# Kernel tuning notes

Hardware: AMD Instinct MI355X
Metric: run time of the kernel (lower is better)

## Reference

```python
import jax, jax.numpy as jnp
import numpy as np

N, E, D_IN, D_OUT = 50000, 1600000, 256, 256


def setup_inputs() -> dict:
    key = jax.random.key(0)
    k1, k2, k3, k4, k5, k6 = jax.random.split(key, 6)
    x = jax.random.normal(k1, (N, D_IN), dtype=jnp.float32)
    edge_index = jax.random.randint(k2, (2, E), 0, N, dtype=jnp.int64)
    s = 1.0 / np.sqrt(D_IN)
    W1 = jax.random.uniform(k3, (D_OUT, D_IN), minval=-s, maxval=s, dtype=jnp.float32)
    b1 = jax.random.uniform(k4, (D_OUT,), minval=-s, maxval=s, dtype=jnp.float32)
    W2 = jax.random.uniform(k5, (D_OUT, D_IN), minval=-s, maxval=s, dtype=jnp.float32)
    b2 = jax.random.uniform(k6, (D_OUT,), minval=-s, maxval=s, dtype=jnp.float32)
    return {"x": x, "W1": W1, "b1": b1, "W2": W2, "b2": b2, "edge_index": edge_index}


def reference(x, W1, b1, W2, b2, edge_index):
    # edge_index[0] = destination node, edge_index[1] = neighbor (as in the torch loop)
    dst = edge_index[0]
    nbr = edge_index[1]
    n = x.shape[0]
    # segment mean of neighbor features per destination node
    agg = jax.ops.segment_sum(x[nbr], dst, num_segments=n)  # [N, D_IN]
    cnt = jax.ops.segment_sum(jnp.ones((nbr.shape[0],), x.dtype), dst, num_segments=n)
    mean = agg / jnp.maximum(cnt, 1.0)[:, None]  # isolated nodes -> 0 (torch gives NaN)
    return x @ W1.T + b1 + mean @ W2.T + b2
```

## Files before the change

kernel.cpp:

```cpp
#include <hip/hip_runtime.h>
#include <hip/hip_bf16.h>
#include <hip/hip_fp8.h>

typedef __bf16 bf16x4 __attribute__((ext_vector_type(4)));
typedef __bf16 bf16x8 __attribute__((ext_vector_type(8)));
typedef float f32x4 __attribute__((ext_vector_type(4)));
typedef float f32x2 __attribute__((ext_vector_type(2)));

#define D_IN 256
#define D_OUT 256
#define K_DIM 512
#define PAD 96
#define NBIN 640
#define NPS 79
#define ROUND1 3072
#define CAP3 20
#define CVT_BLK 1024
#define CONVW_BLK 512


__device__ __forceinline__ unsigned int pack4_fp8(float a, float b, float c, float d) {
#if __has_builtin(__builtin_amdgcn_cvt_pk_fp8_f32)
    int r = 0;
    r = __builtin_amdgcn_cvt_pk_fp8_f32(a, b, r, false);
    r = __builtin_amdgcn_cvt_pk_fp8_f32(c, d, r, true);
    return (unsigned int)r;
#else
    union { unsigned int u; unsigned char by[4]; } v;
    v.by[0] = __hip_fp8_e4m3(a).__x;
    v.by[1] = __hip_fp8_e4m3(b).__x;
    v.by[2] = __hip_fp8_e4m3(c).__x;
    v.by[3] = __hip_fp8_e4m3(d).__x;
    return v.u;
#endif
}

__device__ __forceinline__ void unpack4_fp8(unsigned int u, f32x2& lo, f32x2& hi) {
#if __has_builtin(__builtin_amdgcn_cvt_pk_f32_fp8)
    lo = __builtin_amdgcn_cvt_pk_f32_fp8(u, false);
    hi = __builtin_amdgcn_cvt_pk_f32_fp8(u, true);
#else
    union { unsigned int uu; unsigned char by[4]; } v; v.uu = u;
    __hip_fp8_e4m3 q0, q1, q2, q3;
    q0.__x = v.by[0]; q1.__x = v.by[1]; q2.__x = v.by[2]; q3.__x = v.by[3];
    lo[0] = (float)q0; lo[1] = (float)q1; hi[0] = (float)q2; hi[1] = (float)q3;
#endif
}


__global__ __launch_bounds__(256) void prep_kernel(const int* __restrict__ dst,
                                                   unsigned int* __restrict__ hist,
                                                   const float* __restrict__ x,
                                                   unsigned int* __restrict__ x8,
                                                   __bf16* __restrict__ xb,
                                                   const float* __restrict__ W1,
                                                   const float* __restrict__ W2,
                                                   const float* __restrict__ b1,
                                                   const float* __restrict__ b2,
                                                   __bf16* __restrict__ Wbuf,
                                                   float* __restrict__ bias,
                                                   int E, int n8, int nSub) {
    __shared__ int bcnt[NBIN];
    const int tid = threadIdx.x;
    const int bid = blockIdx.x;

    if (bid < nSub) {
        for (int s = tid; s < NBIN; s += 256) bcnt[s] = 0;
        __syncthreads();
        const int base = bid * ROUND1;
        const int hi = min(E, base + ROUND1);
        for (int e = base + tid; e < hi; e += 256) {
            int d = __builtin_nontemporal_load(dst + e);
            atomicAdd(&bcnt[d / NPS], 1);
        }
        __syncthreads();
        for (int s = tid; s < NBIN; s += 256)
            hist[(size_t)bid * NBIN + s] = (unsigned int)bcnt[s];
    } else if (bid < nSub + CVT_BLK) {
        int i = (bid - nSub) * 256 + tid;
        for (; i < n8; i += CVT_BLK * 256) {
            const float4* p = (const float4*)(x + (size_t)i * 8);
            float4 a = p[0], b = p[1];
            uint2 o;
            o.x = pack4_fp8(a.x, a.y, a.z, a.w);
            o.y = pack4_fp8(b.x, b.y, b.z, b.w);
            *(uint2*)(x8 + (size_t)i * 2) = o;
            bf16x8 hb = { (__bf16)a.x, (__bf16)a.y, (__bf16)a.z, (__bf16)a.w,
                          (__bf16)b.x, (__bf16)b.y, (__bf16)b.z, (__bf16)b.w };
            *(bf16x8*)(xb + (size_t)i * 8) = hb;
        }
    } else {
        int i = (bid - nSub - CVT_BLK) * 256 + tid;
        int o = i >> 9;
        int k = i & 511;
        float v = (k < D_IN) ? W1[o * D_IN + k] : W2[o * D_IN + (k - D_IN)];
        Wbuf[i] = (__bf16)v;
        if (i < D_OUT) bias[i] = b1[i] + b2[i];
    }
}


__global__ __launch_bounds__(64) void scan_kernel(const unsigned int* __restrict__ hist,
                                                  unsigned int* __restrict__ sbase,
                                                  int* __restrict__ bin_cnt, int nSub) {
    const int s = blockIdx.x;
    const int lane = threadIdx.x;
    unsigned int carry = 0;
    for (int b0 = 0; b0 < nSub; b0 += 64) {
        int b = b0 + lane;
        unsigned int v = (b < nSub) ? hist[(size_t)b * NBIN + s] : 0u;
        unsigned int sc = v;
        #pragma unroll
        for (int d = 1; d < 64; d <<= 1) {
            unsigned int t = __shfl_up(sc, d, 64);
            if (lane >= d) sc += t;
        }
        if (b < nSub) sbase[(size_t)b * NBIN + s] = carry + sc - v;
        carry += __shfl(sc, 63, 64);
    }
    if (lane == 0) bin_cnt[s] = (int)carry;
}


__global__ __launch_bounds__(256) void place_kernel(const int* __restrict__ dst,
                                                    const int* __restrict__ nbr,
                                                    const unsigned int* __restrict__ sbase,
                                                    unsigned int* __restrict__ bins,
                                                    int E, int segCap, int nSub) {
    __shared__ unsigned int buf[NBIN][CAP3];
    __shared__ int bcnt[NBIN];
    __shared__ unsigned int gbase[NBIN];
    const int tid = threadIdx.x;
    const int bid = blockIdx.x;

    for (int s = tid; s < NBIN; s += 256) {
        bcnt[s] = 0;
        gbase[s] = sbase[(size_t)bid * NBIN + s];
    }
    __syncthreads();

    const int base = bid * ROUND1;
    const int hi = min(E, base + ROUND1);
    for (int e = base + tid; e < hi; e += 256) {
        int d  = __builtin_nontemporal_load(dst + e);
        int nb = __builtin_nontemporal_load(nbr + e);
        int s = d / NPS;
        unsigned int packed = ((unsigned int)d << 16) | (unsigned int)nb;
        int pos = atomicAdd(&bcnt[s], 1);
        if (pos < CAP3) buf[s][pos] = packed;
        else bins[(size_t)s * segCap + gbase[s] + pos] = packed;
    }
    __syncthreads();

    const int wave = tid >> 6, lane = tid & 63;
    for (int s = wave; s < NBIN; s += 4) {
        int c = min(bcnt[s], CAP3);
        if (lane < c) bins[(size_t)s * segCap + gbase[s] + lane] = buf[s][lane];
    }
}


__global__ __launch_bounds__(512) void fillgather_kernel(const unsigned int* __restrict__ x8,
                                                         const unsigned int* __restrict__ bins,
                                                         const int* __restrict__ bin_cnt,
                                                         __bf16* __restrict__ Mbuf,
                                                         int segCap, int N) {
    __shared__ unsigned short lbuck[NPS][PAD];
    __shared__ int lcnt[NPS];
    const int s = blockIdx.x;
    const int node0 = s * NPS;
    const int tid = threadIdx.x;

    for (int i = tid; i < NPS; i += 512) lcnt[i] = 0;
    __syncthreads();

    const int cnt = min(bin_cnt[s], segCap);
    const size_t sbase_ = (size_t)s * segCap;
    for (int i = tid; i < cnt; i += 512) {
        unsigned int p = bins[sbase_ + i];
        int nl = (int)(p >> 16) - node0;
        int pos = atomicAdd(&lcnt[nl], 1);
        if (pos < PAD) lbuck[nl][pos] = (unsigned short)(p & 0xffffu);
    }
    __syncthreads();

    const int wave = tid >> 6, lane = tid & 63;
    for (int nl = wave; nl < NPS; nl += 8) {
        int node = node0 + nl;
        if (node >= N) continue;
        int c = min(lcnt[nl], PAD);
        const unsigned int* bw = (const unsigned int*)(&lbuck[nl][0]);

        f32x2 a0lo = {0.f,0.f}, a0hi = {0.f,0.f};
        f32x2 a1lo = {0.f,0.f}, a1hi = {0.f,0.f};
        f32x2 a2lo = {0.f,0.f}, a2hi = {0.f,0.f};
        f32x2 a3lo = {0.f,0.f}, a3hi = {0.f,0.f};

        int i = 0;
        for (; i + 16 <= c; i += 16) {
            int ib = i >> 1;
            unsigned int w0 = bw[ib+0], w1 = bw[ib+1], w2 = bw[ib+2], w3 = bw[ib+3];
            unsigned int w4 = bw[ib+4], w5 = bw[ib+5], w6 = bw[ib+6], w7 = bw[ib+7];
            unsigned int u0  = x8[(size_t)(w0 & 0xffffu) * 64 + lane];
            unsigned int u1  = x8[(size_t)(w0 >> 16)     * 64 + lane];
            unsigned int u2  = x8[(size_t)(w1 & 0xffffu) * 64 + lane];
            unsigned int u3  = x8[(size_t)(w1 >> 16)     * 64 + lane];
            unsigned int u4  = x8[(size_t)(w2 & 0xffffu) * 64 + lane];
            unsigned int u5  = x8[(size_t)(w2 >> 16)     * 64 + lane];
            unsigned int u6  = x8[(size_t)(w3 & 0xffffu) * 64 + lane];
            unsigned int u7  = x8[(size_t)(w3 >> 16)     * 64 + lane];
            unsigned int u8  = x8[(size_t)(w4 & 0xffffu) * 64 + lane];
            unsigned int u9  = x8[(size_t)(w4 >> 16)     * 64 + lane];
            unsigned int u10 = x8[(size_t)(w5 & 0xffffu) * 64 + lane];
            unsigned int u11 = x8[(size_t)(w5 >> 16)     * 64 + lane];
            unsigned int u12 = x8[(size_t)(w6 & 0xffffu) * 64 + lane];
            unsigned int u13 = x8[(size_t)(w6 >> 16)     * 64 + lane];
            unsigned int u14 = x8[(size_t)(w7 & 0xffffu) * 64 + lane];
            unsigned int u15 = x8[(size_t)(w7 >> 16)     * 64 + lane];
            f32x2 lo, hi;
            unpack4_fp8(u0,  lo, hi); a0lo += lo; a0hi += hi;
            unpack4_fp8(u1,  lo, hi); a1lo += lo; a1hi += hi;
            unpack4_fp8(u2,  lo, hi); a2lo += lo; a2hi += hi;
            unpack4_fp8(u3,  lo, hi); a3lo += lo; a3hi += hi;
            unpack4_fp8(u4,  lo, hi); a0lo += lo; a0hi += hi;
            unpack4_fp8(u5,  lo, hi); a1lo += lo; a1hi += hi;
            unpack4_fp8(u6,  lo, hi); a2lo += lo; a2hi += hi;
            unpack4_fp8(u7,  lo, hi); a3lo += lo; a3hi += hi;
            unpack4_fp8(u8,  lo, hi); a0lo += lo; a0hi += hi;
            unpack4_fp8(u9,  lo, hi); a1lo += lo; a1hi += hi;
            unpack4_fp8(u10, lo, hi); a2lo += lo; a2hi += hi;
            unpack4_fp8(u11, lo, hi); a3lo += lo; a3hi += hi;
            unpack4_fp8(u12, lo, hi); a0lo += lo; a0hi += hi;
            unpack4_fp8(u13, lo, hi); a1lo += lo; a1hi += hi;
            unpack4_fp8(u14, lo, hi); a2lo += lo; a2hi += hi;
            unpack4_fp8(u15, lo, hi); a3lo += lo; a3hi += hi;
        }
        for (; i + 4 <= c; i += 4) {
            int ib = i >> 1;
            unsigned int w0 = bw[ib+0], w1 = bw[ib+1];
            unsigned int u0 = x8[(size_t)(w0 & 0xffffu) * 64 + lane];
            unsigned int u1 = x8[(size_t)(w0 >> 16)     * 64 + lane];
            unsigned int u2 = x8[(size_t)(w1 & 0xffffu) * 64 + lane];
            unsigned int u3 = x8[(size_t)(w1 >> 16)     * 64 + lane];
            f32x2 lo, hi;
            unpack4_fp8(u0, lo, hi); a0lo += lo; a0hi += hi;
            unpack4_fp8(u1, lo, hi); a1lo += lo; a1hi += hi;
            unpack4_fp8(u2, lo, hi); a2lo += lo; a2hi += hi;
            unpack4_fp8(u3, lo, hi); a3lo += lo; a3hi += hi;
        }
        for (; i < c; i++) {
            unsigned int u0 = x8[(size_t)lbuck[nl][i] * 64 + lane];
            f32x2 lo, hi;
            unpack4_fp8(u0, lo, hi); a0lo += lo; a0hi += hi;
        }
        a0lo += a1lo + a2lo + a3lo;
        a0hi += a1hi + a2hi + a3hi;
        float inv = (c > 0) ? 1.0f / (float)c : 0.0f;
        bf16x4 hm = { (__bf16)(a0lo[0] * inv), (__bf16)(a0lo[1] * inv),
                      (__bf16)(a0hi[0] * inv), (__bf16)(a0hi[1] * inv) };
        *(bf16x4*)(Mbuf + (size_t)node * D_IN + lane * 4) = hm;
    }
}


__global__ __launch_bounds__(512, 5) void gemm_kernel(const __bf16* __restrict__ xb,
                                                      const __bf16* __restrict__ Mb,
                                                      const __bf16* __restrict__ W,
                                                      const float* __restrict__ bias,
                                                      float* __restrict__ out, int M) {
    __shared__ __bf16 As[64][40];
    __shared__ __bf16 Ws[256][40];

    const int tid = threadIdx.x;
    const int lane = tid & 63;
    const int wave = tid >> 6;
    const int wr = wave >> 2;
    const int wc = wave & 3;
    const int brow = blockIdx.x * 64;

    f32x4 acc[2][4];
    #pragma unroll
    for (int m = 0; m < 2; m++)
        #pragma unroll
        for (int n = 0; n < 4; n++)
            acc[m][n] = (f32x4){0.f, 0.f, 0.f, 0.f};

    const int lr = lane & 15;
    const int lg8 = (lane >> 4) * 8;

    const int rowA = tid >> 2;
    const int chA  = (tid & 3) * 8;
    const int growA = brow + rowA;
    const bool aOK = (tid < 256) && (growA < M);
    const int rowW0 = tid >> 2;
    const int rowW1 = (512 + tid) >> 2;
    const int chW = (tid & 3) * 8;

    bf16x8 rA = {};
    bf16x8 rW0, rW1;

    if (aOK) rA = *(const bf16x8*)(xb + (size_t)growA * D_IN + chA);
    rW0 = *(const bf16x8*)(W + (size_t)rowW0 * K_DIM + chW);
    rW1 = *(const bf16x8*)(W + (size_t)rowW1 * K_DIM + chW);

    for (int kk = 0; kk < 16; kk++) {
        if (tid < 256) *(bf16x8*)(&As[rowA][chA]) = rA;
        *(bf16x8*)(&Ws[rowW0][chW]) = rW0;
        *(bf16x8*)(&Ws[rowW1][chW]) = rW1;
        __syncthreads();

        if (kk < 15) {
            const int kn = (kk + 1) * 32;
            const __bf16* srcA = (kn < D_IN) ? xb : Mb;
            if (aOK) rA = *(const bf16x8*)(srcA + (size_t)growA * D_IN + (kn & (D_IN - 1)) + chA);
            rW0 = *(const bf16x8*)(W + (size_t)rowW0 * K_DIM + kn + chW);
            rW1 = *(const bf16x8*)(W + (size_t)rowW1 * K_DIM + kn + chW);
        }

        bf16x8 af[2], wf[4];
        #pragma unroll
        for (int m = 0; m < 2; m++) af[m] = *(const bf16x8*)(&As[wr * 32 + m * 16 + lr][lg8]);
        #pragma unroll
        for (int n = 0; n < 4; n++) wf[n] = *(const bf16x8*)(&Ws[wc * 64 + n * 16 + lr][lg8]);

        #pragma unroll
        for (int m = 0; m < 2; m++)
            #pragma unroll
            for (int n = 0; n < 4; n++)
                acc[m][n] = __builtin_amdgcn_mfma_f32_16x16x32_bf16(af[m], wf[n], acc[m][n], 0, 0, 0);
        __syncthreads();
    }

    const int lg = lane >> 4;
    #pragma unroll
    for (int nf = 0; nf < 4; nf++) {
        int col = wc * 64 + nf * 16 + lr;
        float bv = bias[col];
        #pragma unroll
        for (int mf = 0; mf < 2; mf++) {
            int row0 = brow + wr * 32 + mf * 16 + lg * 4;
            #pragma unroll
            for (int j = 0; j < 4; j++) {
                int row = row0 + j;
                if (row < M) out[(size_t)row * D_OUT + col] = acc[mf][nf][j] + bv;
            }
        }
    }
}


extern "C" void kernel_launch(void* const* d_in, const int* in_sizes, int n_in,
                              void* d_out, int out_size, void* d_ws, size_t ws_size,
                              hipStream_t stream) {
    const float* x  = (const float*)d_in[0];
    const float* W1 = (const float*)d_in[1];
    const float* b1 = (const float*)d_in[2];
    const float* W2 = (const float*)d_in[3];
    const float* b2 = (const float*)d_in[4];
    const int* edges = (const int*)d_in[5];

    const int N = in_sizes[0] / D_IN;
    const int E = in_sizes[5] / 2;
    const int* dst = edges;
    const int* nbr = edges + E;
    const int segCap = (E / NBIN) * 3 / 2 + 64;
    const int nSub = (E + ROUND1 - 1) / ROUND1;
    const int n8 = N * D_IN / 8;

    char* ws = (char*)d_ws;
    size_t woff = 0;
    auto alloc = [&](size_t bytes) -> void* {
        void* p = ws + woff;
        woff = (woff + bytes + 255) & ~(size_t)255;
        return p;
    };
    unsigned int* x8 = (unsigned int*)alloc((size_t)N * D_IN);
    __bf16* xb   = (__bf16*)alloc((size_t)N * D_IN * 2);
    __bf16* Mbuf = (__bf16*)alloc((size_t)N * D_IN * 2);
    __bf16* Wbuf = (__bf16*)alloc((size_t)D_OUT * K_DIM * 2);
    float*  bias = (float*)alloc(D_OUT * 4);
    int* bin_cnt = (int*)alloc(NBIN * 4);
    unsigned int* hist  = (unsigned int*)alloc((size_t)nSub * NBIN * 4);
    unsigned int* sbase = (unsigned int*)alloc((size_t)nSub * NBIN * 4);
    unsigned int* bins  = (unsigned int*)alloc((size_t)NBIN * segCap * 4);

    prep_kernel<<<nSub + CVT_BLK + CONVW_BLK, 256, 0, stream>>>(
        dst, hist, x, x8, xb, W1, W2, b1, b2, Wbuf, bias, E, n8, nSub);
    scan_kernel<<<NBIN, 64, 0, stream>>>(hist, sbase, bin_cnt, nSub);
    place_kernel<<<nSub, 256, 0, stream>>>(dst, nbr, sbase, bins, E, segCap, nSub);

    int fgBlocks = (N + NPS - 1) / NPS;
    fillgather_kernel<<<fgBlocks, 512, 0, stream>>>(x8, bins, bin_cnt, Mbuf, segCap, N);

    int nblk = (N + 63) / 64;
    gemm_kernel<<<nblk, 512, 0, stream>>>(xb, Mbuf, Wbuf, bias, (float*)d_out, N);
}
```

Before: 170.7 us.

## Split GEMM and overlap x@W1 half with edge placement in one launch

Splits the fused K=512 GEMM into two halves. The x@W1 half (plus bias) runs as extra blocks inside the edge-placement kernel, so the dense matmul overlaps with the memory-bound scatter. The mean@W2 half runs after the gather and accumulates into the output by read-modify-write. The placement path moves to 512 threads with a smaller per-bin LDS buffer (CAP3 20->12) so both roles fit one shared-memory layout, at the cost of an extra pass reading and writing the output.

```diff
diff --git a/kernel.cpp b/kernel.cpp
--- a/kernel.cpp
+++ b/kernel.cpp
@@ -14,7 +14,7 @@
 #define NBIN 640
 #define NPS 79
 #define ROUND1 3072
-#define CAP3 20
+#define CAP3 12
 #define CVT_BLK 1024
 #define CONVW_BLK 512
 
@@ -122,40 +122,125 @@
 }
 
 
-__global__ __launch_bounds__(256) void place_kernel(const int* __restrict__ dst,
-                                                    const int* __restrict__ nbr,
-                                                    const unsigned int* __restrict__ sbase,
-                                                    unsigned int* __restrict__ bins,
-                                                    int E, int segCap, int nSub) {
-    __shared__ unsigned int buf[NBIN][CAP3];
-    __shared__ int bcnt[NBIN];
-    __shared__ unsigned int gbase[NBIN];
+__global__ __launch_bounds__(512) void placegemm1_kernel(const int* __restrict__ dst,
+                                                         const int* __restrict__ nbr,
+                                                         const unsigned int* __restrict__ sbase,
+                                                         unsigned int* __restrict__ bins,
+                                                         const __bf16* __restrict__ xb,
+                                                         const __bf16* __restrict__ W,
+                                                         const float* __restrict__ bias,
+                                                         float* __restrict__ out,
+                                                         int E, int segCap, int nSub,
+                                                         int M, int g1) {
+    __shared__ __align__(16) char smem[35840];
     const int tid = threadIdx.x;
     const int bid = blockIdx.x;
 
-    for (int s = tid; s < NBIN; s += 256) {
-        bcnt[s] = 0;
-        gbase[s] = sbase[(size_t)bid * NBIN + s];
-    }
-    __syncthreads();
-
-    const int base = bid * ROUND1;
-    const int hi = min(E, base + ROUND1);
-    for (int e = base + tid; e < hi; e += 256) {
-        int d  = __builtin_nontemporal_load(dst + e);
-        int nb = __builtin_nontemporal_load(nbr + e);
-        int s = d / NPS;
-        unsigned int packed = ((unsigned int)d << 16) | (unsigned int)nb;
-        int pos = atomicAdd(&bcnt[s], 1);
-        if (pos < CAP3) buf[s][pos] = packed;
-        else bins[(size_t)s * segCap + gbase[s] + pos] = packed;
-    }
-    __syncthreads();
-
-    const int wave = tid >> 6, lane = tid & 63;
-    for (int s = wave; s < NBIN; s += 4) {
-        int c = min(bcnt[s], CAP3);
-        if (lane < c) bins[(size_t)s * segCap + gbase[s] + lane] = buf[s][lane];
+    if (bid < g1) {
+        __bf16 (*As)[40] = (__bf16(*)[40])smem;
+        __bf16 (*Ws)[40] = (__bf16(*)[40])(smem + 5120);
+
+        const int lane = tid & 63;
+        const int wave = tid >> 6;
+        const int wr = wave >> 2;
+        const int wc = wave & 3;
+        const int brow = bid * 64;
+
+        f32x4 acc[2][4];
+        #pragma unroll
+        for (int m = 0; m < 2; m++)
+            #pragma unroll
+            for (int n = 0; n < 4; n++)
+                acc[m][n] = (f32x4){0.f, 0.f, 0.f, 0.f};
+
+        const int lr = lane & 15;
+        const int lg8 = (lane >> 4) * 8;
+        const int rowA = tid >> 2;
+        const int chA  = (tid & 3) * 8;
+        const int growA = brow + rowA;
+        const bool aOK = (tid < 256) && (growA < M);
+        const int rowW0 = tid >> 2;
+        const int rowW1 = (512 + tid) >> 2;
+        const int chW = (tid & 3) * 8;
+
+        bf16x8 rA = {};
+        bf16x8 rW0, rW1;
+        if (aOK) rA = *(const bf16x8*)(xb + (size_t)growA * D_IN + chA);
+        rW0 = *(const bf16x8*)(W + (size_t)rowW0 * K_DIM + chW);
+        rW1 = *(const bf16x8*)(W + (size_t)rowW1 * K_DIM + chW);
+
+        for (int kk = 0; kk < 8; kk++) {
+            if (tid < 256) *(bf16x8*)(&As[rowA][chA]) = rA;
+            *(bf16x8*)(&Ws[rowW0][chW]) = rW0;
+            *(bf16x8*)(&Ws[rowW1][chW]) = rW1;
+            __syncthreads();
+
+            if (kk < 7) {
+                const int kn = (kk + 1) * 32;
+                if (aOK) rA = *(const bf16x8*)(xb + (size_t)growA * D_IN + kn + chA);
+                rW0 = *(const bf16x8*)(W + (size_t)rowW0 * K_DIM + kn + chW);
+                rW1 = *(const bf16x8*)(W + (size_t)rowW1 * K_DIM + kn + chW);
+            }
+
+            bf16x8 af[2], wf[4];
+            #pragma unroll
+            for (int m = 0; m < 2; m++) af[m] = *(const bf16x8*)(&As[wr * 32 + m * 16 + lr][lg8]);
+            #pragma unroll
+            for (int n = 0; n < 4; n++) wf[n] = *(const bf16x8*)(&Ws[wc * 64 + n * 16 + lr][lg8]);
+
+            #pragma unroll
+            for (int m = 0; m < 2; m++)
+                #pragma unroll
+                for (int n = 0; n < 4; n++)
+                    acc[m][n] = __builtin_amdgcn_mfma_f32_16x16x32_bf16(af[m], wf[n], acc[m][n], 0, 0, 0);
+            __syncthreads();
+        }
+
+        const int lg = lane >> 4;
+        #pragma unroll
+        for (int nf = 0; nf < 4; nf++) {
+            int col = wc * 64 + nf * 16 + lr;
+            float bv = bias[col];
+            #pragma unroll
+            for (int mf = 0; mf < 2; mf++) {
+                int row0 = brow + wr * 32 + mf * 16 + lg * 4;
+                #pragma unroll
+                for (int j = 0; j < 4; j++) {
+                    int row = row0 + j;
+                    if (row < M) out[(size_t)row * D_OUT + col] = acc[mf][nf][j] + bv;
+                }
+            }
+        }
+    } else {
+        unsigned int (*buf)[CAP3] = (unsigned int(*)[CAP3])smem;
+        int* bcnt = (int*)(smem + 30720);
+        unsigned int* gbase = (unsigned int*)(smem + 33280);
+        const int pbid = bid - g1;
+
+        for (int s = tid; s < NBIN; s += 512) {
+            bcnt[s] = 0;
+            gbase[s] = sbase[(size_t)pbid * NBIN + s];
+        }
+        __syncthreads();
+
+        const int base = pbid * ROUND1;
+        const int hi = min(E, base + ROUND1);
+        for (int e = base + tid; e < hi; e += 512) {
+            int d  = __builtin_nontemporal_load(dst + e);
+            int nb = __builtin_nontemporal_load(nbr + e);
+            int s = d / NPS;
+            unsigned int packed = ((unsigned int)d << 16) | (unsigned int)nb;
+            int pos = atomicAdd(&bcnt[s], 1);
+            if (pos < CAP3) buf[s][pos] = packed;
+            else bins[(size_t)s * segCap + gbase[s] + pos] = packed;
+        }
+        __syncthreads();
+
+        const int wave = tid >> 6, lane = tid & 63;
+        for (int s = wave; s < NBIN; s += 8) {
+            int c = min(bcnt[s], CAP3);
+            if (lane < c) bins[(size_t)s * segCap + gbase[s] + lane] = buf[s][lane];
+        }
     }
 }
 
@@ -263,11 +348,9 @@
 }
 
 
-__global__ __launch_bounds__(512, 5) void gemm_kernel(const __bf16* __restrict__ xb,
-                                                      const __bf16* __restrict__ Mb,
-                                                      const __bf16* __restrict__ W,
-                                                      const float* __restrict__ bias,
-                                                      float* __restrict__ out, int M) {
+__global__ __launch_bounds__(512, 5) void gemm2_kernel(const __bf16* __restrict__ Mb,
+                                                       const __bf16* __restrict__ W,
+                                                       float* __restrict__ out, int M) {
     __shared__ __bf16 As[64][40];
     __shared__ __bf16 Ws[256][40];
 
@@ -287,7 +370,6 @@
 
     const int lr = lane & 15;
     const int lg8 = (lane >> 4) * 8;
-
     const int rowA = tid >> 2;
     const int chA  = (tid & 3) * 8;
     const int growA = brow + rowA;
@@ -298,23 +380,21 @@
 
     bf16x8 rA = {};
     bf16x8 rW0, rW1;
-
-    if (aOK) rA = *(const bf16x8*)(xb + (size_t)growA * D_IN + chA);
-    rW0 = *(const bf16x8*)(W + (size_t)rowW0 * K_DIM + chW);
-    rW1 = *(const bf16x8*)(W + (size_t)rowW1 * K_DIM + chW);
-
-    for (int kk = 0; kk < 16; kk++) {
+    if (aOK) rA = *(const bf16x8*)(Mb + (size_t)growA * D_IN + chA);
+    rW0 = *(const bf16x8*)(W + (size_t)rowW0 * K_DIM + D_IN + chW);
+    rW1 = *(const bf16x8*)(W + (size_t)rowW1 * K_DIM + D_IN + chW);
+
+    for (int kk = 0; kk < 8; kk++) {
         if (tid < 256) *(bf16x8*)(&As[rowA][chA]) = rA;
         *(bf16x8*)(&Ws[rowW0][chW]) = rW0;
         *(bf16x8*)(&Ws[rowW1][chW]) = rW1;
         __syncthreads();
 
-        if (kk < 15) {
+        if (kk < 7) {
             const int kn = (kk + 1) * 32;
-            const __bf16* srcA = (kn < D_IN) ? xb : Mb;
-            if (aOK) rA = *(const bf16x8*)(srcA + (size_t)growA * D_IN + (kn & (D_IN - 1)) + chA);
-            rW0 = *(const bf16x8*)(W + (size_t)rowW0 * K_DIM + kn + chW);
-            rW1 = *(const bf16x8*)(W + (size_t)rowW1 * K_DIM + kn + chW);
+            if (aOK) rA = *(const bf16x8*)(Mb + (size_t)growA * D_IN + kn + chA);
+            rW0 = *(const bf16x8*)(W + (size_t)rowW0 * K_DIM + D_IN + kn + chW);
+            rW1 = *(const bf16x8*)(W + (size_t)rowW1 * K_DIM + D_IN + kn + chW);
         }
 
         bf16x8 af[2], wf[4];
@@ -335,14 +415,16 @@
     #pragma unroll
     for (int nf = 0; nf < 4; nf++) {
         int col = wc * 64 + nf * 16 + lr;
-        float bv = bias[col];
         #pragma unroll
         for (int mf = 0; mf < 2; mf++) {
             int row0 = brow + wr * 32 + mf * 16 + lg * 4;
             #pragma unroll
             for (int j = 0; j < 4; j++) {
                 int row = row0 + j;
-                if (row < M) out[(size_t)row * D_OUT + col] = acc[mf][nf][j] + bv;
+                if (row < M) {
+                    size_t idx = (size_t)row * D_OUT + col;
+                    out[idx] = out[idx] + acc[mf][nf][j];
+                }
             }
         }
     }
@@ -387,11 +469,13 @@
     prep_kernel<<<nSub + CVT_BLK + CONVW_BLK, 256, 0, stream>>>(
         dst, hist, x, x8, xb, W1, W2, b1, b2, Wbuf, bias, E, n8, nSub);
     scan_kernel<<<NBIN, 64, 0, stream>>>(hist, sbase, bin_cnt, nSub);
-    place_kernel<<<nSub, 256, 0, stream>>>(dst, nbr, sbase, bins, E, segCap, nSub);
+
+    const int g1 = (N + 63) / 64;
+    placegemm1_kernel<<<g1 + nSub, 512, 0, stream>>>(
+        dst, nbr, sbase, bins, xb, Wbuf, bias, (float*)d_out, E, segCap, nSub, N, g1);
 
     int fgBlocks = (N + NPS - 1) / NPS;
     fillgather_kernel<<<fgBlocks, 512, 0, stream>>>(x8, bins, bin_cnt, Mbuf, segCap, N);
 
-    int nblk = (N + 63) / 64;
-    gemm_kernel<<<nblk, 512, 0, stream>>>(xb, Mbuf, Wbuf, bias, (float*)d_out, N);
-}
+    gemm2_kernel<<<g1, 512, 0, stream>>>(Mbuf, Wbuf, (float*)d_out, N);
+}
```

Result: no change. 167.9 us (-1.7%).

## Drop LDS staging in GEMM, load MFMA fragments directly; widen place kernel

Applied to the files above, without the earlier changes.

The GEMM kernel stops staging A and W tiles through shared memory with barriers. Each wave now loads its MFMA fragments straight from global memory, relying on L1/L2 for reuse of W across blocks and waves. This removes LDS traffic and __syncthreads, but adds redundant global loads of W and drops the register prefetch pipeline. Separately, place_kernel runs with 512 threads and a smaller per-bin LDS buffer (CAP3 12), meant to raise occupancy at the cost of more direct global scatter writes.

```diff
diff --git a/kernel.cpp b/kernel.cpp
--- a/kernel.cpp
+++ b/kernel.cpp
@@ -14,7 +14,7 @@
 #define NBIN 640
 #define NPS 79
 #define ROUND1 3072
-#define CAP3 20
+#define CAP3 12
 #define CVT_BLK 1024
 #define CONVW_BLK 512
 
@@ -122,7 +122,7 @@
 }
 
 
-__global__ __launch_bounds__(256) void place_kernel(const int* __restrict__ dst,
+__global__ __launch_bounds__(512) void place_kernel(const int* __restrict__ dst,
                                                     const int* __restrict__ nbr,
                                                     const unsigned int* __restrict__ sbase,
                                                     unsigned int* __restrict__ bins,
@@ -133,7 +133,7 @@
     const int tid = threadIdx.x;
     const int bid = blockIdx.x;
 
-    for (int s = tid; s < NBIN; s += 256) {
+    for (int s = tid; s < NBIN; s += 512) {
         bcnt[s] = 0;
         gbase[s] = sbase[(size_t)bid * NBIN + s];
     }
@@ -141,7 +141,7 @@
 
     const int base = bid * ROUND1;
     const int hi = min(E, base + ROUND1);
-    for (int e = base + tid; e < hi; e += 256) {
+    for (int e = base + tid; e < hi; e += 512) {
         int d  = __builtin_nontemporal_load(dst + e);
         int nb = __builtin_nontemporal_load(nbr + e);
         int s = d / NPS;
@@ -153,7 +153,7 @@
     __syncthreads();
 
     const int wave = tid >> 6, lane = tid & 63;
-    for (int s = wave; s < NBIN; s += 4) {
+    for (int s = wave; s < NBIN; s += 8) {
         int c = min(bcnt[s], CAP3);
         if (lane < c) bins[(size_t)s * segCap + gbase[s] + lane] = buf[s][lane];
     }
@@ -263,14 +263,11 @@
 }
 
 
-__global__ __launch_bounds__(512, 5) void gemm_kernel(const __bf16* __restrict__ xb,
-                                                      const __bf16* __restrict__ Mb,
-                                                      const __bf16* __restrict__ W,
-                                                      const float* __restrict__ bias,
-                                                      float* __restrict__ out, int M) {
-    __shared__ __bf16 As[64][40];
-    __shared__ __bf16 Ws[256][40];
-
+__global__ __launch_bounds__(512) void gemm_kernel(const __bf16* __restrict__ xb,
+                                                   const __bf16* __restrict__ Mb,
+                                                   const __bf16* __restrict__ W,
+                                                   const float* __restrict__ bias,
+                                                   float* __restrict__ out, int M) {
     const int tid = threadIdx.x;
     const int lane = tid & 63;
     const int wave = tid >> 6;
@@ -278,6 +275,17 @@
     const int wc = wave & 3;
     const int brow = blockIdx.x * 64;
 
+    const int lr = lane & 15;
+    const int lg8 = (lane >> 4) * 8;
+
+    const int r0 = min(brow + wr * 32 + lr, M - 1);
+    const int r1 = min(brow + wr * 32 + 16 + lr, M - 1);
+    const __bf16* a0x = xb + (size_t)r0 * D_IN + lg8;
+    const __bf16* a1x = xb + (size_t)r1 * D_IN + lg8;
+    const __bf16* a0m = Mb + (size_t)r0 * D_IN + lg8;
+    const __bf16* a1m = Mb + (size_t)r1 * D_IN + lg8;
+    const __bf16* wp = W + (size_t)(wc * 64 + lr) * K_DIM + lg8;
+
     f32x4 acc[2][4];
     #pragma unroll
     for (int m = 0; m < 2; m++)
@@ -285,50 +293,41 @@
         for (int n = 0; n < 4; n++)
             acc[m][n] = (f32x4){0.f, 0.f, 0.f, 0.f};
 
-    const int lr = lane & 15;
-    const int lg8 = (lane >> 4) * 8;
-
-    const int rowA = tid >> 2;
-    const int chA  = (tid & 3) * 8;
-    const int growA = brow + rowA;
-    const bool aOK = (tid < 256) && (growA < M);
-    const int rowW0 = tid >> 2;
-    const int rowW1 = (512 + tid) >> 2;
-    const int chW = (tid & 3) * 8;
-
-    bf16x8 rA = {};
-    bf16x8 rW0, rW1;
-
-    if (aOK) rA = *(const bf16x8*)(xb + (size_t)growA * D_IN + chA);
-    rW0 = *(const bf16x8*)(W + (size_t)rowW0 * K_DIM + chW);
-    rW1 = *(const bf16x8*)(W + (size_t)rowW1 * K_DIM + chW);
-
-    for (int kk = 0; kk < 16; kk++) {
-        if (tid < 256) *(bf16x8*)(&As[rowA][chA]) = rA;
-        *(bf16x8*)(&Ws[rowW0][chW]) = rW0;
-        *(bf16x8*)(&Ws[rowW1][chW]) = rW1;
-        __syncthreads();
-
-        if (kk < 15) {
-            const int kn = (kk + 1) * 32;
-            const __bf16* srcA = (kn < D_IN) ? xb : Mb;
-            if (aOK) rA = *(const bf16x8*)(srcA + (size_t)growA * D_IN + (kn & (D_IN - 1)) + chA);
-            rW0 = *(const bf16x8*)(W + (size_t)rowW0 * K_DIM + kn + chW);
-            rW1 = *(const bf16x8*)(W + (size_t)rowW1 * K_DIM + kn + chW);
-        }
-
-        bf16x8 af[2], wf[4];
-        #pragma unroll
-        for (int m = 0; m < 2; m++) af[m] = *(const bf16x8*)(&As[wr * 32 + m * 16 + lr][lg8]);
-        #pragma unroll
-        for (int n = 0; n < 4; n++) wf[n] = *(const bf16x8*)(&Ws[wc * 64 + n * 16 + lr][lg8]);
-
-        #pragma unroll
-        for (int m = 0; m < 2; m++)
-            #pragma unroll
-            for (int n = 0; n < 4; n++)
-                acc[m][n] = __builtin_amdgcn_mfma_f32_16x16x32_bf16(af[m], wf[n], acc[m][n], 0, 0, 0);
-        __syncthreads();
+    #pragma unroll
+    for (int kk = 0; kk < 8; kk++) {
+        const int k0 = kk * 32;
+        bf16x8 af0 = *(const bf16x8*)(a0x + k0);
+        bf16x8 af1 = *(const bf16x8*)(a1x + k0);
+        bf16x8 wf0 = *(const bf16x8*)(wp + k0);
+        bf16x8 wf1 = *(const bf16x8*)(wp + 16 * K_DIM + k0);
+        bf16x8 wf2 = *(const bf16x8*)(wp + 32 * K_DIM + k0);
+        bf16x8 wf3 = *(const bf16x8*)(wp + 48 * K_DIM + k0);
+        acc[0][0] = __builtin_amdgcn_mfma_f32_16x16x32_bf16(af0, wf0, acc[0][0], 0, 0, 0);
+        acc[0][1] = __builtin_amdgcn_mfma_f32_16x16x32_bf16(af0, wf1, acc[0][1], 0, 0, 0);
+        acc[0][2] = __builtin_amdgcn_mfma_f32_16x16x32_bf16(af0, wf2, acc[0][2], 0, 0, 0);
+        acc[0][3] = __builtin_amdgcn_mfma_f32_16x16x32_bf16(af0, wf3, acc[0][3], 0, 0, 0);
+        acc[1][0] = __builtin_amdgcn_mfma_f32_16x16x32_bf16(af1, wf0, acc[1][0], 0, 0, 0);
+        acc[1][1] = __builtin_amdgcn_mfma_f32_16x16x32_bf16(af1, wf1, acc[1][1], 0, 0, 0);
+        acc[1][2] = __builtin_amdgcn_mfma_f32_16x16x32_bf16(af1, wf2, acc[1][2], 0, 0, 0);
+        acc[1][3] = __builtin_amdgcn_mfma_f32_16x16x32_bf16(af1, wf3, acc[1][3], 0, 0, 0);
+    }
+    #pragma unroll
+    for (int kk = 0; kk < 8; kk++) {
+        const int k0 = kk * 32;
+        bf16x8 af0 = *(const bf16x8*)(a0m + k0);
+        bf16x8 af1 = *(const bf16x8*)(a1m + k0);
+        bf16x8 wf0 = *(const bf16x8*)(wp + D_IN + k0);
+        bf16x8 wf1 = *(const bf16x8*)(wp + 16 * K_DIM + D_IN + k0);
+        bf16x8 wf2 = *(const bf16x8*)(wp + 32 * K_DIM + D_IN + k0);
+        bf16x8 wf3 = *(const bf16x8*)(wp + 48 * K_DIM + D_IN + k0);
+        acc[0][0] = __builtin_amdgcn_mfma_f32_16x16x32_bf16(af0, wf0, acc[0][0], 0, 0, 0);
+        acc[0][1] = __builtin_amdgcn_mfma_f32_16x16x32_bf16(af0, wf1, acc[0][1], 0, 0, 0);
+        acc[0][2] = __builtin_amdgcn_mfma_f32_16x16x32_bf16(af0, wf2, acc[0][2], 0, 0, 0);
+        acc[0][3] = __builtin_amdgcn_mfma_f32_16x16x32_bf16(af0, wf3, acc[0][3], 0, 0, 0);
+        acc[1][0] = __builtin_amdgcn_mfma_f32_16x16x32_bf16(af1, wf0, acc[1][0], 0, 0, 0);
+        acc[1][1] = __builtin_amdgcn_mfma_f32_16x16x32_bf16(af1, wf1, acc[1][1], 0, 0, 0);
+        acc[1][2] = __builtin_amdgcn_mfma_f32_16x16x32_bf16(af1, wf2, acc[1][2], 0, 0, 0);
+        acc[1][3] = __builtin_amdgcn_mfma_f32_16x16x32_bf16(af1, wf3, acc[1][3], 0, 0, 0);
     }
 
     const int lg = lane >> 4;
@@ -387,7 +386,7 @@
     prep_kernel<<<nSub + CVT_BLK + CONVW_BLK, 256, 0, stream>>>(
         dst, hist, x, x8, xb, W1, W2, b1, b2, Wbuf, bias, E, n8, nSub);
     scan_kernel<<<NBIN, 64, 0, stream>>>(hist, sbase, bin_cnt, nSub);
-    place_kernel<<<nSub, 256, 0, stream>>>(dst, nbr, sbase, bins, E, segCap, nSub);
+    place_kernel<<<nSub, 512, 0, stream>>>(dst, nbr, sbase, bins, E, segCap, nSub);
 
     int fgBlocks = (N + NPS - 1) / NPS;
     fillgather_kernel<<<fgBlocks, 512, 0, stream>>>(x8, bins, bin_cnt, Mbuf, segCap, N);
```

New measurement: 194.7 us. 14.0% more time.
